# Kernel tuning notes

Hardware: AMD Instinct MI355X
Metric: run time of the kernel (lower is better)

## Reference

```python
import jax, jax.numpy as jnp
import numpy as np

K_NEIGH = 20
GROUPS = 4
KPTS = 9  # 3x3 deformable kernel
FH, FW = 240, 320


def _bn(x, p):
    # p: (4,C) rows = gamma, beta, running_mean, running_var ; x: (B,C,...)
    g, b, m, v = p[0], p[1], p[2], p[3]
    shp = (1, -1) + (1,) * (x.ndim - 2)
    return (x - m.reshape(shp)) * (g.reshape(shp) / jnp.sqrt(v.reshape(shp) + 1e-5)) + b.reshape(shp)


def _lrelu(x):
    return jnp.where(x >= 0, x, 0.2 * x)


def _c1x1(x, w):  # w: (Cout,Cin)
    return jnp.einsum('oc,bc...->bo...', w, x)


def _hswish(x):
    return x * jnp.clip(x + 3.0, 0.0, 6.0) / 6.0


def _coord_att(x, c1w, c1b, bnp, chw, chb, cww, cwb):
    B, C, H, W = x.shape
    ph = x.mean(axis=3, keepdims=True)                              # (B,C,H,1)
    pw = x.mean(axis=2, keepdims=True).transpose(0, 1, 3, 2)        # (B,C,W,1)
    y = jnp.concatenate([ph, pw], axis=2)                           # (B,C,H+W,1)
    y = _hswish(_bn(_c1x1(y, c1w) + c1b.reshape(1, -1, 1, 1), bnp))
    yh, yw = y[:, :, :H], y[:, :, H:]
    ah = jax.nn.sigmoid(_c1x1(yh, chw) + chb.reshape(1, -1, 1, 1))                         # (B,C,H,1)
    aw = jax.nn.sigmoid(_c1x1(yw.transpose(0, 1, 3, 2), cww) + cwb.reshape(1, -1, 1, 1))   # (B,C,1,W)
    return x * ah * aw


def _knn(x, k):
    xx = jnp.sum(x * x, axis=1)                     # (B,N)
    inner = jnp.einsum('bcn,bcm->bnm', x, x)
    pd = 2.0 * inner - xx[:, :, None] - xx[:, None, :]   # negative sq. distance
    return jax.lax.top_k(pd, k)[1]                  # (B,N,k)


def _graph_feature(x, k):
    B, C, N = x.shape
    idx = _knn(x, k)
    xt = x.transpose(0, 2, 1)                       # (B,N,C)
    nb = jax.vmap(lambda a, i: a[i])(xt, idx)       # (B,N,k,C)
    ctr = xt[:, :, None, :]
    f = jnp.concatenate([nb - ctr, jnp.broadcast_to(ctr, (B, N, k, C))], axis=3)
    return f.transpose(0, 3, 1, 2)                  # (B,2C,N,k)


def _dcnv4(x, off_w, off_b, val_w, val_b, out_w, out_b):
    B, C, H, W = x.shape
    Cg = C // GROUPS
    xh = x.transpose(0, 2, 3, 1)                    # (B,H,W,C)
    value = xh @ val_w + val_b
    om = (xh @ off_w + off_b).reshape(B, H, W, GROUPS, KPTS, 3)
    offs, mask = om[..., :2], om[..., 2]            # DCNv4: mask used un-normalized
    ky, kx = jnp.meshgrid(jnp.arange(-1, 2), jnp.arange(-1, 2), indexing='ij')
    kgrid = jnp.stack([kx.ravel(), ky.ravel()], -1).astype(x.dtype)      # (K,2) xy
    gy, gx = jnp.meshgrid(jnp.arange(H), jnp.arange(W), indexing='ij')
    base = jnp.stack([gx, gy], -1).astype(x.dtype)  # (H,W,2)
    loc = base[None, :, :, None, None, :] + kgrid + offs                 # (B,H,W,G,K,2)
    vflat = value.reshape(B, H * W, GROUPS, Cg)
    outs = []
    for g in range(GROUPS):
        lx = loc[:, :, :, g, :, 0]
        ly = loc[:, :, :, g, :, 1]                  # (B,H,W,K)
        x0 = jnp.floor(lx); y0 = jnp.floor(ly)
        wx = lx - x0; wy = ly - y0
        vg = vflat[:, :, g]                         # (B,HW,Cg)
        samp = jnp.zeros((B, H, W, KPTS, Cg), x.dtype)
        for yi, xi, w in ((y0, x0, (1 - wx) * (1 - wy)), (y0, x0 + 1, wx * (1 - wy)),
                          (y0 + 1, x0, (1 - wx) * wy), (y0 + 1, x0 + 1, wx * wy)):
            inb = (yi >= 0) & (yi < H) & (xi >= 0) & (xi < W)
            ii = (jnp.clip(yi, 0, H - 1) * W + jnp.clip(xi, 0, W - 1)).astype(jnp.int32)
            gathered = jax.vmap(lambda v, i: v[i])(vg, ii.reshape(B, -1)).reshape(B, H, W, KPTS, Cg)
            samp = samp + (w * inb)[..., None] * gathered
        outs.append(jnp.einsum('bhwk,bhwkc->bhwc', mask[:, :, :, g], samp))
    out = jnp.concatenate(outs, axis=-1) @ out_w + out_b
    return out.transpose(0, 3, 1, 2)


def setup_inputs() -> dict:
    key = jax.random.key(0)
    ks = jax.random.split(key, 24)
    B, N, IN_CH, FEAT_DIM = 2, 4096, 3, 128
    pc = jax.random.normal(ks[0], (B, 8, N), jnp.float32)
    v = jax.random.uniform(ks[1], (B, 1, N), jnp.float32, -240.0, 240.0)
    u = jax.random.uniform(ks[2], (B, 1, N), jnp.float32, -320.0, 320.0)
    pc = jnp.concatenate([v, u, pc[:, 2:]], axis=1)
    feat_s00 = jax.random.normal(ks[3], (B, IN_CH, 480, 640), jnp.float32)

    def w(k, shape, s=0.05):
        return jax.random.normal(k, shape, jnp.float32) * s

    def bn(c):
        return jnp.stack([jnp.ones(c), jnp.zeros(c), jnp.zeros(c), jnp.ones(c)]).astype(jnp.float32)

    OC = GROUPS * KPTS * 3
    return dict(
        pc_xyzrgb=pc, feat_s00=feat_s00,
        preconv_w=w(ks[4], (24, IN_CH, 3, 3)), preconv_b=jnp.zeros(24, jnp.float32),
        ca_c1_w=w(ks[5], (8, 24)), ca_c1_b=jnp.zeros(8, jnp.float32), ca_bn=bn(8),
        ca_ch_w=w(ks[6], (24, 8)), ca_ch_b=jnp.zeros(24, jnp.float32),
        ca_cw_w=w(ks[7], (24, 8)), ca_cw_b=jnp.zeros(24, jnp.float32),
        conv1_w=w(ks[8], (64, 64)), bn1=bn(64),
        conv2_w=w(ks[9], (64, 128)), bn2=bn(64),
        conv3_w=w(ks[10], (128, 128)), bn3=bn(128),
        lin4a_w=w(ks[11], (256, 256)), lin4b_w=w(ks[12], (256, 64)),
        dcn5_off_w=w(ks[13], (64, OC), 0.01), dcn5_off_b=jnp.zeros(OC, jnp.float32),
        dcn5_val_w=w(ks[14], (64, 64)), dcn5_val_b=jnp.zeros(64, jnp.float32),
        dcn5_out_w=w(ks[15], (64, 64)), dcn5_out_b=jnp.zeros(64, jnp.float32), bn5=bn(64),
        dcn6_off_w=w(ks[16], (64, OC), 0.01), dcn6_off_b=jnp.zeros(OC, jnp.float32),
        dcn6_val_w=w(ks[17], (64, 64)), dcn6_val_b=jnp.zeros(64, jnp.float32),
        dcn6_out_w=w(ks[18], (64, 64)), dcn6_out_b=jnp.zeros(64, jnp.float32), bn6=bn(64),
        conv7a_w=w(ks[19], (64, 64)), conv7b_w=w(ks[20], (FEAT_DIM, 64)),
    )


def reference(pc_xyzrgb, feat_s00, preconv_w, preconv_b, ca_c1_w, ca_c1_b, ca_bn, ca_ch_w, ca_ch_b,
              ca_cw_w, ca_cw_b, conv1_w, bn1, conv2_w, bn2, conv3_w, bn3, lin4a_w, lin4b_w,
              dcn5_off_w, dcn5_off_b, dcn5_val_w, dcn5_val_b, dcn5_out_w, dcn5_out_b, bn5,
              dcn6_off_w, dcn6_off_b, dcn6_val_w, dcn6_val_b, dcn6_out_w, dcn6_out_b, bn6,
              conv7a_w, conv7b_w):
    B, _, N = pc_xyzrgb.shape
    v = jnp.floor(pc_xyzrgb[:, 0] + 240.0).astype(jnp.int32).reshape(-1)
    u = jnp.floor(pc_xyzrgb[:, 1] + 320.0).astype(jnp.int32).reshape(-1)
    bi = jnp.repeat(jnp.arange(B, dtype=jnp.int32), N)
    # preConv: 3x3 conv + CoordAtt, then gather per-point 2D features
    fs1 = jax.lax.conv_general_dilated(feat_s00, preconv_w, (1, 1), 'SAME') + preconv_b.reshape(1, -1, 1, 1)
    fs1 = _coord_att(fs1, ca_c1_w, ca_c1_b, ca_bn, ca_ch_w, ca_ch_b, ca_cw_w, ca_cw_b)
    fs1 = fs1.transpose(0, 2, 3, 1)                                  # (B,480,640,24)
    feat_2d = fs1[bi, v, u].reshape(B, N, 24)
    feat_3d = jnp.concatenate([pc_xyzrgb.transpose(0, 2, 1), feat_2d], axis=2).transpose(0, 2, 1)  # (B,32,N)
    x = _lrelu(_bn(_c1x1(_graph_feature(feat_3d, K_NEIGH), conv1_w), bn1))
    x1 = x.max(axis=-1)                                              # (B,64,N)
    x = _lrelu(_bn(_c1x1(_graph_feature(x1, K_NEIGH), conv2_w), bn2))
    x2 = x.max(axis=-1)
    x = _lrelu(_bn(_c1x1(_graph_feature(x2, K_NEIGH), conv3_w), bn3))
    x3 = x.max(axis=-1)                                              # (B,128,N)
    x = jnp.concatenate([x1, x2, x3], axis=1).transpose(0, 2, 1)     # (B,N,256)
    x = (x @ lin4a_w) @ lin4b_w                                      # (B,N,64)
    fm = jnp.zeros((B, FH, FW, 64), x.dtype).at[bi, v // 2, u // 2].add(x.reshape(B * N, 64))
    fm = jax.nn.softmax(fm.transpose(0, 3, 1, 2), axis=1)            # (B,64,240,320)
    fm = _lrelu(_bn(_dcnv4(fm, dcn5_off_w, dcn5_off_b, dcn5_val_w, dcn5_val_b, dcn5_out_w, dcn5_out_b), bn5))
    fm = _lrelu(_bn(_dcnv4(fm, dcn6_off_w, dcn6_off_b, dcn6_val_w, dcn6_val_b, dcn6_out_w, dcn6_out_b), bn6))
    fm = _c1x1(_c1x1(fm, conv7a_w), conv7b_w)                        # (B,feat_dim,240,320)
    idx1 = jnp.stack([bi, v // 2, u // 2], axis=0)
    return fm, idx1
```

## Files before the change

kernel.cpp:

```cpp
#include <hip/hip_runtime.h>
#include <math.h>

#define B_    2
#define N_    4096
#define BN_   (B_*N_)
#define H0    480
#define W0    640
#define FH_   240
#define FW_   320
#define PIX_  (B_*FH_*FW_)
#define KNN_K 20

static const size_t OFF_RS   = 0;
static const size_t OFF_CS   = 2944;
static const size_t OFF_PH   = 6784;
static const size_t OFF_PW   = 29824;
static const size_t OFF_Y8   = 60544;
static const size_t OFF_AH   = 78464;
static const size_t OFF_AW   = 101504;
static const size_t OFF_VB   = 132224;
static const size_t OFF_UB   = 140416;
static const size_t OFF_F3D  = 148608;
static const size_t OFF_XX   = 410752;
static const size_t OFF_IDX  = 5661824;
static const size_t OFF_X1   = 5825664;
static const size_t OFF_X2   = 6349952;
static const size_t OFF_X3   = 6874240;
static const size_t OFF_T1   = 7922816;
static const size_t OFF_T2   = 7926912;
static const size_t OFF_T3   = 7935104;
static const size_t OFF_T7A  = 7951488;
static const size_t OFF_T7B  = 7955584;
static const size_t OFF_FMA  = 7963776;
static const size_t OFF_FMV  = 17794176;
static const size_t OFF_FMB  = 27624576;

__global__ void k_transpose(const float* __restrict__ w1, const float* __restrict__ w2,
                            const float* __restrict__ w3, const float* __restrict__ w7a,
                            const float* __restrict__ w7b,
                            float* __restrict__ t1, float* __restrict__ t2,
                            float* __restrict__ t3, float* __restrict__ t7a,
                            float* __restrict__ t7b) {
    int t = blockIdx.x * 256 + threadIdx.x;
    if (t < 4096) {
        int i = t >> 6, o = t & 63; t1[i*64+o] = w1[o*64+i];
    } else if (t < 12288) {
        int r = t - 4096; int i = r >> 6, o = r & 63; t2[i*64+o] = w2[o*128+i];
    } else if (t < 28672) {
        int r = t - 12288; int i = r >> 7, o = r & 127; t3[i*128+o] = w3[o*128+i];
    } else if (t < 32768) {
        int r = t - 28672; int c = r >> 6, o = r & 63; t7a[c*64+o] = w7a[o*64+c];
    } else if (t < 40960) {
        int r = t - 32768; int o = r >> 7, p = r & 127; t7b[o*128+p] = w7b[p*64+o];
    }
}

__global__ void k_sums(const float* __restrict__ img, float* __restrict__ cs,
                       float* __restrict__ rs) {
    int t = blockIdx.x * 256 + threadIdx.x;
    if (t < 6*W0) {
        int bc = t / W0, x = t % W0;
        const float* p = img + (size_t)bc * H0 * W0;
        float acc = 0.f;
        for (int h = 0; h < H0; ++h) acc += p[h * W0 + x];
        cs[bc * W0 + x] = acc;
    } else {
        int t2 = t - 6*W0;
        if (t2 < 6*H0) {
            int bc = t2 / H0, y = t2 % H0;
            const float* p = img + (size_t)bc * H0 * W0 + (size_t)y * W0;
            float acc = 0.f;
            for (int x = 0; x < W0; ++x) acc += p[x];
            rs[bc * H0 + y] = acc;
        }
    }
}

__global__ void k_phpw(const float* __restrict__ img, const float* __restrict__ rs,
                       const float* __restrict__ cs, const float* __restrict__ w,
                       const float* __restrict__ bias,
                       float* __restrict__ ph, float* __restrict__ pw) {
    int t = blockIdx.x * 256 + threadIdx.x;
    if (t < B_ * 24 * H0) {
        int h = t % H0; int bc = t / H0; int c = bc % 24; int b = bc / 24;
        float acc = 0.f;
        for (int ic = 0; ic < 3; ++ic)
            for (int dy = 0; dy < 3; ++dy) {
                int y = h + dy - 1;
                if ((unsigned)y >= (unsigned)H0) continue;
                float r = rs[(b*3+ic)*H0 + y];
                const float* row = img + (size_t)((b*3+ic)*H0 + y) * W0;
                float e0 = row[0], eL = row[W0-1];
                const float* wp = w + ((c*3+ic)*3+dy)*3;
                acc += wp[0]*(r - eL) + wp[1]*r + wp[2]*(r - e0);
            }
        ph[t] = bias[c] + acc / 640.0f;
    } else {
        int t2 = t - B_ * 24 * H0;
        if (t2 < B_ * 24 * W0) {
            int x = t2 % W0; int bc = t2 / W0; int c = bc % 24; int b = bc / 24;
            float acc = 0.f;
            for (int ic = 0; ic < 3; ++ic)
                for (int dx = 0; dx < 3; ++dx) {
                    int xx = x + dx - 1;
                    if ((unsigned)xx >= (unsigned)W0) continue;
                    float csv = cs[(b*3+ic)*W0 + xx];
                    const float* base = img + (size_t)(b*3+ic) * H0 * W0;
                    float top = base[xx];
                    float bot = base[(size_t)(H0-1)*W0 + xx];
                    const float* wp = w + ((c*3+ic)*3)*3 + dx;
                    acc += wp[0]*(csv - bot) + wp[3]*csv + wp[6]*(csv - top);
                }
            pw[t2] = bias[c] + acc / 480.0f;
        }
    }
}

__global__ void k_y8ahw(const float* __restrict__ ph, const float* __restrict__ pw,
                        const float* __restrict__ c1w, const float* __restrict__ c1b,
                        const float* __restrict__ bnp,
                        const float* __restrict__ chw, const float* __restrict__ chb,
                        const float* __restrict__ cww, const float* __restrict__ cwb,
                        float* __restrict__ ah, float* __restrict__ aw) {
    int t = blockIdx.x * 256 + threadIdx.x;
    if (t >= B_ * 1120) return;
    int pos = t % 1120; int b = t / 1120;
    float yv[24];
#pragma unroll
    for (int c = 0; c < 24; ++c)
        yv[c] = (pos < H0) ? ph[(b*24+c)*H0 + pos] : pw[(b*24+c)*W0 + (pos - H0)];
    float y8j[8];
#pragma unroll
    for (int j = 0; j < 8; ++j) {
        float s = c1b[j];
#pragma unroll
        for (int c = 0; c < 24; ++c) s = fmaf(c1w[j*24+c], yv[c], s);
        float g = bnp[j], be = bnp[8+j], m = bnp[16+j], va = bnp[24+j];
        float v = (s - m) * (g / sqrtf(va + 1e-5f)) + be;
        y8j[j] = v * fminf(fmaxf(v + 3.f, 0.f), 6.f) * (1.f/6.f);
    }
    if (pos < H0) {
#pragma unroll
        for (int c = 0; c < 24; ++c) {
            float s = chb[c];
#pragma unroll
            for (int j = 0; j < 8; ++j) s = fmaf(chw[c*8+j], y8j[j], s);
            ah[(b*24+c)*H0 + pos] = 1.f / (1.f + expf(-s));
        }
    } else {
#pragma unroll
        for (int c = 0; c < 24; ++c) {
            float s = cwb[c];
#pragma unroll
            for (int j = 0; j < 8; ++j) s = fmaf(cww[c*8+j], y8j[j], s);
            aw[(b*24+c)*W0 + (pos - H0)] = 1.f / (1.f + expf(-s));
        }
    }
}

__global__ void k_feat3d(const float* __restrict__ pc, const float* __restrict__ img,
                         const float* __restrict__ w, const float* __restrict__ bias,
                         const float* __restrict__ ah, const float* __restrict__ aw,
                         float* __restrict__ f3d, int* __restrict__ vbuf,
                         int* __restrict__ ubuf, float* __restrict__ idx_out) {
    int t = blockIdx.x * 256 + threadIdx.x;
    if (t >= BN_ * 32) return;
    int c = t & 31; int bn = t >> 5; int b = bn >> 12; int n = bn & (N_-1);
    float pv = pc[(b*8 + 0)*N_ + n];
    float pu = pc[(b*8 + 1)*N_ + n];
    int v = (int)floorf(pv + 240.f);
    int u = (int)floorf(pu + 320.f);
    float f;
    if (c < 8) {
        f = pc[(b*8 + c)*N_ + n];
    } else {
        int co = c - 8;
        float acc = bias[co];
        for (int ic = 0; ic < 3; ++ic)
            for (int dy = 0; dy < 3; ++dy) {
                int y = v + dy - 1;
                if ((unsigned)y >= (unsigned)H0) continue;
                for (int dx = 0; dx < 3; ++dx) {
                    int x = u + dx - 1;
                    if ((unsigned)x >= (unsigned)W0) continue;
                    acc = fmaf(w[((co*3+ic)*3+dy)*3+dx],
                               img[((size_t)(b*3+ic)*H0 + y)*W0 + x], acc);
                }
            }
        f = acc * ah[(b*24+co)*H0 + v] * aw[(b*24+co)*W0 + u];
    }
    f3d[(size_t)bn*32 + c] = f;
    if (c == 0) {
        vbuf[bn] = v; ubuf[bn] = u;
        idx_out[bn] = (float)b;
        idx_out[BN_ + bn] = (float)(v >> 1);
        idx_out[2*BN_ + bn] = (float)(u >> 1);
    }
}

template<int C>
__launch_bounds__(256, 2)
__global__ void k_dist(const float* __restrict__ X, float* __restrict__ pd, int b) {
    __shared__ float As[C*128];
    __shared__ float Bs[C*128];
    __shared__ float sXX[256];
    int tid = threadIdx.x;
    int t = blockIdx.x;
    int I = (int)((-1.0f + sqrtf(1.0f + 8.0f*(float)t)) * 0.5f);
    while ((I*(I+1))/2 > t) --I;
    while (((I+1)*(I+2))/2 <= t) ++I;
    int J = t - (I*(I+1))/2;
    {
        int r = tid >> 1, c0 = (tid & 1) * (C/2);
        const float* qa = X + ((size_t)(b*N_ + I*128 + r)) * C + c0;
        const float* ca = X + ((size_t)(b*N_ + J*128 + r)) * C + c0;
#pragma unroll
        for (int m = 0; m < C/8; ++m) {
            float4 va = *(const float4*)(qa + m*4);
            float4 vb = *(const float4*)(ca + m*4);
            int c = c0 + m*4;
            As[(c+0)*128+r]=va.x; As[(c+1)*128+r]=va.y; As[(c+2)*128+r]=va.z; As[(c+3)*128+r]=va.w;
            Bs[(c+0)*128+r]=vb.x; Bs[(c+1)*128+r]=vb.y; Bs[(c+2)*128+r]=vb.z; Bs[(c+3)*128+r]=vb.w;
        }
    }
    __syncthreads();
    int tx = tid & 15, ty = tid >> 4;
    float acc[8][8];
#pragma unroll
    for (int i=0;i<8;++i)
#pragma unroll
        for (int j=0;j<8;++j) acc[i][j]=0.f;
    for (int k = 0; k < C; ++k) {
        float4 a0 = *(const float4*)&As[k*128 + ty*8];
        float4 a1 = *(const float4*)&As[k*128 + ty*8 + 4];
        float4 b0 = *(const float4*)&Bs[k*128 + tx*8];
        float4 b1 = *(const float4*)&Bs[k*128 + tx*8 + 4];
        float av[8] = {a0.x,a0.y,a0.z,a0.w,a1.x,a1.y,a1.z,a1.w};
        float bv[8] = {b0.x,b0.y,b0.z,b0.w,b1.x,b1.y,b1.z,b1.w};
#pragma unroll
        for (int i = 0; i < 8; ++i)
#pragma unroll
            for (int j = 0; j < 8; ++j)
                acc[i][j] = fmaf(av[i], bv[j], acc[i][j]);
    }
    {
        float nacc = 0.f;
        if (tid < 128) {
            for (int c = 0; c < C; ++c) {
                float v = As[c*128 + tid];
                nacc = fmaf(v, v, nacc);
            }
        } else {
            int r = tid - 128;
            for (int c = 0; c < C; ++c) {
                float v = Bs[c*128 + r];
                nacc = fmaf(v, v, nacc);
            }
        }
        sXX[tid] = nacc;
    }
    __syncthreads();
    float xq[8], xc[8];
#pragma unroll
    for (int i = 0; i < 8; ++i) {
        xq[i] = sXX[ty*8 + i];
        xc[i] = sXX[128 + tx*8 + i];
    }
#pragma unroll
    for (int i = 0; i < 8; ++i) {
        int row = I*128 + ty*8 + i;
        float4 o0, o1;
        o0.x = 2.f*acc[i][0] - xq[i] - xc[0]; o0.y = 2.f*acc[i][1] - xq[i] - xc[1];
        o0.z = 2.f*acc[i][2] - xq[i] - xc[2]; o0.w = 2.f*acc[i][3] - xq[i] - xc[3];
        o1.x = 2.f*acc[i][4] - xq[i] - xc[4]; o1.y = 2.f*acc[i][5] - xq[i] - xc[5];
        o1.z = 2.f*acc[i][6] - xq[i] - xc[6]; o1.w = 2.f*acc[i][7] - xq[i] - xc[7];
        *(float4*)&pd[(size_t)row*N_ + J*128 + tx*8]     = o0;
        *(float4*)&pd[(size_t)row*N_ + J*128 + tx*8 + 4] = o1;
    }
    if (I != J) {
#pragma unroll
        for (int j = 0; j < 8; ++j) {
            int row = J*128 + tx*8 + j;
            float4 m0, m1;
            m0.x = 2.f*acc[0][j] - xc[j] - xq[0]; m0.y = 2.f*acc[1][j] - xc[j] - xq[1];
            m0.z = 2.f*acc[2][j] - xc[j] - xq[2]; m0.w = 2.f*acc[3][j] - xc[j] - xq[3];
            m1.x = 2.f*acc[4][j] - xc[j] - xq[4]; m1.y = 2.f*acc[5][j] - xc[j] - xq[5];
            m1.z = 2.f*acc[6][j] - xc[j] - xq[6]; m1.w = 2.f*acc[7][j] - xc[j] - xq[7];
            *(float4*)&pd[(size_t)row*N_ + I*128 + ty*8]     = m0;
            *(float4*)&pd[(size_t)row*N_ + I*128 + ty*8 + 4] = m1;
        }
    }
}

__launch_bounds__(256)
__global__ void k_select(const float* __restrict__ pd, int* __restrict__ idxb, int b) {
    int wv = threadIdx.x >> 6, lane = threadIdx.x & 63;
    int q = blockIdx.x * 4 + wv;
    const float* row = pd + (size_t)q * N_;
    float val[12]; int idx[12];
#pragma unroll
    for (int j = 0; j < 12; ++j) { val[j] = -INFINITY; idx[j] = 0x7fffffff; }
    for (int t = 0; t < N_ / 256; ++t) {
        float4 v4 = *(const float4*)(row + t * 256 + lane * 4);
        float vv[4] = {v4.x, v4.y, v4.z, v4.w};
#pragma unroll
        for (int j = 0; j < 4; ++j) {
            float v = vv[j];
            if (v > val[11]) {
                float cv = v; int cc = t * 256 + lane * 4 + j; bool ins = false;
#pragma unroll
                for (int s = 0; s < 12; ++s) {
                    bool sw = ins || (cv > val[s]);
                    if (sw) {
                        float tv = val[s]; val[s] = cv; cv = tv;
                        int ti = idx[s]; idx[s] = cc; cc = ti;
                        ins = true;
                    }
                }
            }
        }
    }
    int nb = 0;
    float hv = val[0]; int hi = idx[0];
#pragma unroll 1
    for (int slot = 0; slot < KNN_K; ++slot) {
        float wvv = hv; int wi = hi; int wl = lane;
#pragma unroll
        for (int off = 1; off < 64; off <<= 1) {
            float ov = __shfl_xor(wvv, off);
            int   oi = __shfl_xor(wi, off);
            int   ol = __shfl_xor(wl, off);
            bool take = (ov > wvv) || (ov == wvv && oi < wi);
            if (take) { wvv = ov; wi = oi; wl = ol; }
        }
        if (lane == slot) nb = wi;
        bool pop = (lane == wl);
#pragma unroll
        for (int s = 0; s < 11; ++s)
            if (pop) { val[s] = val[s+1]; idx[s] = idx[s+1]; }
        if (pop) { val[11] = -INFINITY; idx[11] = 0x7fffffff; }
        hv = val[0]; hi = idx[0];
    }
    if (lane < KNN_K) idxb[(size_t)(b * N_ + q) * KNN_K + lane] = nb;
}

template<int CIN, int COUT, int P>
__launch_bounds__(256, 2)
__global__ void edgeconv(const float* __restrict__ X, const int* __restrict__ idxb,
                         const float* __restrict__ wT, const float* __restrict__ bnp,
                         float* __restrict__ Y) {
    __shared__ float sctr[P][CIN];
    __shared__ float snb[P][KNN_K * CIN];
    int base = blockIdx.x * P;
    int tid = threadIdx.x;
    const int CIN4 = CIN / 4;
    if (tid < P * CIN4) {
        int p = tid / CIN4, i4 = tid % CIN4;
        ((float4*)sctr[p])[i4] = ((const float4*)&X[(size_t)(base + p) * CIN])[i4];
    }
    for (int j = tid; j < P * KNN_K * CIN4; j += 256) {
        int r = j / CIN4, i4 = j % CIN4;
        int p = r / KNN_K, k = r % KNN_K;
        int b = (base + p) / N_;
        int ni = idxb[(size_t)(base + p) * KNN_K + k];
        ((float4*)snb[p])[k * CIN4 + i4] =
            ((const float4*)&X[((size_t)b * N_ + ni) * CIN])[i4];
    }
    __syncthreads();
    int p = tid / COUT, o = tid % COUT;
    float wreg[CIN];
#pragma unroll
    for (int i = 0; i < CIN; ++i) wreg[i] = wT[i * COUT + o];
    float g = bnp[o], bb = bnp[COUT + o], m = bnp[2*COUT + o], va = bnp[3*COUT + o];
    float a = g / sqrtf(va + 1e-5f);
    float sh = bb - m * a;
    float accc = 0.f;
#pragma unroll
    for (int i = 0; i < CIN; ++i)
        accc = fmaf(wT[(CIN + i) * COUT + o] - wreg[i], sctr[p][i], accc);
    float mx = -INFINITY;
    for (int k = 0; k < KNN_K; ++k) {
        const float4* nb4 = (const float4*)&snb[p][k * CIN];
        float s = accc;
#pragma unroll
        for (int i4 = 0; i4 < CIN4; ++i4) {
            float4 v = nb4[i4];
            s = fmaf(wreg[4*i4+0], v.x, s);
            s = fmaf(wreg[4*i4+1], v.y, s);
            s = fmaf(wreg[4*i4+2], v.z, s);
            s = fmaf(wreg[4*i4+3], v.w, s);
        }
        float r = fmaf(s, a, sh);
        r = (r >= 0.f) ? r : 0.2f * r;
        mx = fmaxf(mx, r);
    }
    Y[(size_t)(base + p) * COUT + o] = mx;
}

__launch_bounds__(256)
__global__ void k_lin4(const float* __restrict__ x1, const float* __restrict__ x2,
                       const float* __restrict__ x3, const float* __restrict__ l4a,
                       const float* __restrict__ l4b, const int* __restrict__ vbuf,
                       const int* __restrict__ ubuf, float* __restrict__ fmA) {
    int p0 = blockIdx.x * 4; int tid = threadIdx.x;
    __shared__ float xc[4][256]; __shared__ float t1s[4][256];
    for (int j = tid; j < 1024; j += 256) {
        int p = j >> 8, i = j & 255;
        int bn = p0 + p;
        float v;
        if (i < 64)       v = x1[(size_t)bn*64 + i];
        else if (i < 128) v = x2[(size_t)bn*64 + i - 64];
        else              v = x3[(size_t)bn*128 + i - 128];
        xc[p][i] = v;
    }
    __syncthreads();
    float acc[4] = {0.f, 0.f, 0.f, 0.f};
#pragma unroll 8
    for (int i = 0; i < 256; ++i) {
        float wv = l4a[i*256 + tid];
#pragma unroll
        for (int p = 0; p < 4; ++p) acc[p] = fmaf(xc[p][i], wv, acc[p]);
    }
#pragma unroll
    for (int p = 0; p < 4; ++p) t1s[p][tid] = acc[p];
    __syncthreads();
    int o = tid & 63, pg = tid >> 6;
    float a2 = 0.f;
#pragma unroll 8
    for (int i = 0; i < 256; ++i) a2 = fmaf(t1s[pg][i], l4b[i*64 + o], a2);
    int bn = p0 + pg;
    int b = bn >> 12; int v = vbuf[bn] >> 1; int u = ubuf[bn] >> 1;
    atomicAdd(fmA + ((size_t)(b*FH_ + v)*FW_ + u)*64 + o, a2);
}

__launch_bounds__(256)
__global__ void k_dcnval(const float* __restrict__ in, const float* __restrict__ vw,
                         const float* __restrict__ vb, float* __restrict__ val,
                         float* __restrict__ smout, int do_sm) {
    __shared__ float sx[8][64];
    int tid = threadIdx.x;
    size_t base = (size_t)blockIdx.x * 512;
    if (tid < 128) ((float4*)sx)[tid] = *((const float4*)(in + base) + tid);
    __syncthreads();
    int o = tid & 63; int pg = tid >> 6;
    if (do_sm) {
        float x0 = sx[pg][o], x1 = sx[pg+4][o];
        float m0 = x0, m1 = x1;
        for (int off = 32; off > 0; off >>= 1) {
            m0 = fmaxf(m0, __shfl_xor(m0, off));
            m1 = fmaxf(m1, __shfl_xor(m1, off));
        }
        float e0 = expf(x0 - m0), e1 = expf(x1 - m1);
        float s0 = e0, s1 = e1;
        for (int off = 32; off > 0; off >>= 1) {
            s0 += __shfl_xor(s0, off);
            s1 += __shfl_xor(s1, off);
        }
        float r0 = e0 / s0, r1 = e1 / s1;
        smout[base + (size_t)pg*64 + o]     = r0;
        smout[base + (size_t)(pg+4)*64 + o] = r1;
        sx[pg][o] = r0; sx[pg+4][o] = r1;
        __syncthreads();
    }
    float bias = vb[o];
    float a0 = 0.f, a1 = 0.f;
#pragma unroll
    for (int i4 = 0; i4 < 16; ++i4) {
        float4 x0 = *(const float4*)&sx[pg][i4*4];
        float4 x1 = *(const float4*)&sx[pg+4][i4*4];
        float w0 = vw[(i4*4+0)*64 + o], w1 = vw[(i4*4+1)*64 + o];
        float w2 = vw[(i4*4+2)*64 + o], w3 = vw[(i4*4+3)*64 + o];
        a0 = fmaf(x0.x,w0,a0); a0 = fmaf(x0.y,w1,a0); a0 = fmaf(x0.z,w2,a0); a0 = fmaf(x0.w,w3,a0);
        a1 = fmaf(x1.x,w0,a1); a1 = fmaf(x1.y,w1,a1); a1 = fmaf(x1.z,w2,a1); a1 = fmaf(x1.w,w3,a1);
    }
    val[base + (size_t)pg*64 + o]     = a0 + bias;
    val[base + (size_t)(pg+4)*64 + o] = a1 + bias;
}

__launch_bounds__(256, 5)
__global__ void k_dcn64(const float* __restrict__ in, const float* __restrict__ val,
                        const float* __restrict__ ow, const float* __restrict__ ob,
                        const float* __restrict__ pwm, const float* __restrict__ pbm,
                        const float* __restrict__ bnp, float* __restrict__ out) {
    __shared__ float xT[64*36];
    __shared__ float somU[64*68];
    __shared__ float stapA[4][40][8];
    int tid = threadIdx.x;
    int blk = blockIdx.x;
    int b = blk / 2400;
    int hw0 = (blk % 2400) * 32;
    size_t pix0 = (size_t)b * (FH_*FW_) + hw0;

    {
        int px = tid >> 3, c0 = (tid & 7) * 8;
        const float* ip = in + (pix0 + px) * 64 + c0;
#pragma unroll
        for (int m = 0; m < 2; ++m) {
            float4 v = *(const float4*)(ip + m*4);
            int c = c0 + m*4;
            xT[(c+0)*36 + px] = v.x; xT[(c+1)*36 + px] = v.y;
            xT[(c+2)*36 + px] = v.z; xT[(c+3)*36 + px] = v.w;
        }
    }
    __builtin_amdgcn_wave_barrier();

    {
        int tx = tid & 15, ty = tid >> 4;
        int oadr[7];
#pragma unroll
        for (int j = 0; j < 7; ++j) {
            int o = tx + 16*j;
            oadr[j] = (o < 108) ? o : 107;
        }
        float acc[2][7];
#pragma unroll
        for (int i=0;i<2;++i)
#pragma unroll
            for (int j=0;j<7;++j) acc[i][j]=0.f;
        for (int c = 0; c < 64; ++c) {
            float2 a = *(const float2*)&xT[c*36 + ty*2];
            const float* owc = ow + c*108;
            float bv[7];
#pragma unroll
            for (int j = 0; j < 7; ++j) bv[j] = owc[oadr[j]];
#pragma unroll
            for (int j = 0; j < 7; ++j) {
                acc[0][j] = fmaf(a.x, bv[j], acc[0][j]);
                acc[1][j] = fmaf(a.y, bv[j], acc[1][j]);
            }
        }
#pragma unroll
        for (int j = 0; j < 7; ++j) {
            int o = tx + 16*j;
            if (o < 108) {
                float bias = ob[o];
                somU[(ty*2+0)*113 + o] = acc[0][j] + bias;
                somU[(ty*2+1)*113 + o] = acc[1][j] + bias;
            }
        }
    }
    __builtin_amdgcn_wave_barrier();

    int wv = tid >> 6, lane = tid & 63;
    const float* vb0 = val + (size_t)b * (FH_*FW_) * 64;
    int lane4 = lane << 2;
    for (int j = 0; j < 8; ++j) {
        int px = wv*8 + j;
        if (lane < 36) {
            int g = lane / 9, k = lane % 9;
            int hw = hw0 + px;
            int h = hw / FW_, w = hw % FW_;
            float lx = (float)(w + (k%3) - 1) + somU[px*113 + g*27 + k*3 + 0];
            float ly = (float)(h + (k/3) - 1) + somU[px*113 + g*27 + k*3 + 1];
            float msk = somU[px*113 + g*27 + k*3 + 2];
            float x0f = floorf(lx), y0f = floorf(ly);
            float wx = lx - x0f, wy = ly - y0f;
            int x0 = (int)x0f, y0 = (int)y0f;
            bool xi0 = (unsigned)x0 < (unsigned)FW_, xi1 = (unsigned)(x0+1) < (unsigned)FW_;
            bool yi0 = (unsigned)y0 < (unsigned)FH_, yi1 = (unsigned)(y0+1) < (unsigned)FH_;
            int x0c = min(max(x0, 0), FW_-1), x1c = min(max(x0+1, 0), FW_-1);
            int y0c = min(max(y0, 0), FH_-1), y1c = min(max(y0+1, 0), FH_-1);
            float4 fA, fW;
            fA.x = __int_as_float((y0c*FW_ + x0c) << 8);
            fA.y = __int_as_float((y0c*FW_ + x1c) << 8);
            fA.z = __int_as_float((y1c*FW_ + x0c) << 8);
            fA.w = __int_as_float((y1c*FW_ + x1c) << 8);
            fW.x = (xi0 && yi0) ? msk*(1.f-wx)*(1.f-wy) : 0.f;
            fW.y = (xi1 && yi0) ? msk*wx*(1.f-wy)       : 0.f;
            fW.z = (xi0 && yi1) ? msk*(1.f-wx)*wy       : 0.f;
            fW.w = (xi1 && yi1) ? msk*wx*wy             : 0.f;
            *(float4*)&stapA[wv][lane][0] = fA;
            *(float4*)&stapA[wv][lane][4] = fW;
        }
        __builtin_amdgcn_wave_barrier();
        {
            int g9 = (lane >> 4) * 9;
            float acc0 = 0.f, acc1 = 0.f;
#pragma unroll
            for (int k = 0; k < 9; ++k) {
                float4 A = *(const float4*)&stapA[wv][g9 + k][0];
                float4 W = *(const float4*)&stapA[wv][g9 + k][4];
                int a00 = __float_as_int(A.x) + lane4;
                int a01 = __float_as_int(A.y) + lane4;
                int a10 = __float_as_int(A.z) + lane4;
                int a11 = __float_as_int(A.w) + lane4;
                float v00 = *(const float*)((const char*)vb0 + (unsigned)a00);
                float v01 = *(const float*)((const char*)vb0 + (unsigned)a01);
                float v10 = *(const float*)((const char*)vb0 + (unsigned)a10);
                float v11 = *(const float*)((const char*)vb0 + (unsigned)a11);
                acc0 = fmaf(W.x, v00, acc0);
                acc1 = fmaf(W.y, v01, acc1);
                acc0 = fmaf(W.z, v10, acc0);
                acc1 = fmaf(W.w, v11, acc1);
            }
            xT[lane*36 + px] = acc0 + acc1;
        }
        __builtin_amdgcn_wave_barrier();
    }

    __syncthreads();
    for (int m = 0; m < 4; ++m) {
        int idx = tid + 256*m;
        int c = idx >> 4, o4 = (idx & 15) * 4;
        float4 v = *(const float4*)(pwm + c*64 + o4);
        *(float4*)&somU[c*68 + o4] = v;
    }
    __syncthreads();

    {
        int tx = tid & 15, ty = tid >> 4;
        float acc[2][4];
#pragma unroll
        for (int i=0;i<2;++i)
#pragma unroll
            for (int j=0;j<4;++j) acc[i][j]=0.f;
        for (int c = 0; c < 64; ++c) {
            float2 a = *(const float2*)&xT[c*36 + ty*2];
            float4 bb = *(const float4*)&somU[c*68 + tx*4];
            acc[0][0] = fmaf(a.x, bb.x, acc[0][0]);
            acc[0][1] = fmaf(a.x, bb.y, acc[0][1]);
            acc[0][2] = fmaf(a.x, bb.z, acc[0][2]);
            acc[0][3] = fmaf(a.x, bb.w, acc[0][3]);
            acc[1][0] = fmaf(a.y, bb.x, acc[1][0]);
            acc[1][1] = fmaf(a.y, bb.y, acc[1][1]);
            acc[1][2] = fmaf(a.y, bb.z, acc[1][2]);
            acc[1][3] = fmaf(a.y, bb.w, acc[1][3]);
        }
#pragma unroll
        for (int i = 0; i < 2; ++i) {
            int px = ty*2 + i;
            float vr[4];
#pragma unroll
            for (int jj = 0; jj < 4; ++jj) {
                int o = tx*4 + jj;
                float aa = acc[i][jj] + pbm[o];
                float g = bnp[o], be = bnp[64+o], m = bnp[128+o], va = bnp[192+o];
                float sc = g / sqrtf(va + 1e-5f);
                float r = (aa - m) * sc + be;
                vr[jj] = (r >= 0.f) ? r : 0.2f * r;
            }
            *(float4*)&out[(pix0 + px)*64 + tx*4] = make_float4(vr[0],vr[1],vr[2],vr[3]);
        }
    }
}

__launch_bounds__(256)
__global__ void k_conv7(const float* __restrict__ in, const float* __restrict__ w7aT,
                        const float* __restrict__ w7bT, float* __restrict__ out) {
    int blk = blockIdx.x;
    int b = blk / ((FH_*FW_)/16);
    int hw0 = (blk % ((FH_*FW_)/16)) * 16;
    int tid = threadIdx.x;
    __shared__ float sx[16][64];
    __shared__ float st[16][64];
    for (int j = tid; j < 1024; j += 256) {
        int p = j >> 6, c = j & 63;
        sx[p][c] = in[((size_t)(b*(FH_*FW_) + hw0 + p))*64 + c];
    }
    __syncthreads();
    {
        int o = tid & 63, p4 = tid >> 6;
        float acc[4] = {0.f, 0.f, 0.f, 0.f};
#pragma unroll 8
        for (int c = 0; c < 64; ++c) {
            float wv = w7aT[c*64 + o];
#pragma unroll
            for (int j = 0; j < 4; ++j) acc[j] = fmaf(sx[p4*4+j][c], wv, acc[j]);
        }
#pragma unroll
        for (int j = 0; j < 4; ++j) st[p4*4+j][o] = acc[j];
    }
    __syncthreads();
    {
        int po = tid >> 1, half = tid & 1;
        float acc[8] = {0.f};
#pragma unroll 8
        for (int c = 0; c < 64; ++c) {
            float wv = w7bT[c*128 + po];
#pragma unroll
            for (int j = 0; j < 8; ++j) acc[j] = fmaf(st[half*8+j][c], wv, acc[j]);
        }
        float* op = out + ((size_t)b*128 + po)*(FH_*FW_) + hw0 + half*8;
        *(float4*)op       = make_float4(acc[0], acc[1], acc[2], acc[3]);
        *(float4*)(op + 4) = make_float4(acc[4], acc[5], acc[6], acc[7]);
    }
}

extern "C" void kernel_launch(void* const* d_in, const int* in_sizes, int n_in,
                              void* d_out, int out_size, void* d_ws, size_t ws_size,
                              hipStream_t stream) {
    (void)in_sizes; (void)n_in; (void)out_size; (void)ws_size;
    const float* pc   = (const float*)d_in[0];
    const float* img  = (const float*)d_in[1];
    const float* pcw  = (const float*)d_in[2];
    const float* pcb  = (const float*)d_in[3];
    const float* c1w  = (const float*)d_in[4];
    const float* c1b  = (const float*)d_in[5];
    const float* cabn = (const float*)d_in[6];
    const float* chw  = (const float*)d_in[7];
    const float* chb  = (const float*)d_in[8];
    const float* cww  = (const float*)d_in[9];
    const float* cwb  = (const float*)d_in[10];
    const float* w1   = (const float*)d_in[11];
    const float* bn1  = (const float*)d_in[12];
    const float* w2   = (const float*)d_in[13];
    const float* bn2  = (const float*)d_in[14];
    const float* w3   = (const float*)d_in[15];
    const float* bn3  = (const float*)d_in[16];
    const float* l4a  = (const float*)d_in[17];
    const float* l4b  = (const float*)d_in[18];
    const float* d5ow = (const float*)d_in[19];
    const float* d5ob = (const float*)d_in[20];
    const float* d5vw = (const float*)d_in[21];
    const float* d5vb = (const float*)d_in[22];
    const float* d5pw = (const float*)d_in[23];
    const float* d5pb = (const float*)d_in[24];
    const float* bn5  = (const float*)d_in[25];
    const float* d6ow = (const float*)d_in[26];
    const float* d6ob = (const float*)d_in[27];
    const float* d6vw = (const float*)d_in[28];
    const float* d6vb = (const float*)d_in[29];
    const float* d6pw = (const float*)d_in[30];
    const float* d6pb = (const float*)d_in[31];
    const float* bn6  = (const float*)d_in[32];
    const float* w7a  = (const float*)d_in[33];
    const float* w7b  = (const float*)d_in[34];

    float* ws  = (float*)d_ws;
    float* out = (float*)d_out;

    float* rs  = ws + OFF_RS;   float* cs  = ws + OFF_CS;
    float* ph  = ws + OFF_PH;   float* pw  = ws + OFF_PW;
    float* ah  = ws + OFF_AH;   float* aw  = ws + OFF_AW;
    int*   vb  = (int*)(ws + OFF_VB);
    int*   ub  = (int*)(ws + OFF_UB);
    float* f3d = ws + OFF_F3D;
    int*   idxb = (int*)(ws + OFF_IDX);
    float* x1  = ws + OFF_X1;   float* x2  = ws + OFF_X2;  float* x3 = ws + OFF_X3;
    float* t1  = ws + OFF_T1;   float* t2  = ws + OFF_T2;  float* t3 = ws + OFF_T3;
    float* t7a = ws + OFF_T7A;  float* t7b = ws + OFF_T7B;
    float* fmA = ws + OFF_FMA;  float* fmV = ws + OFF_FMV; float* fmB = ws + OFF_FMB;
    float* pdb = ws + OFF_FMA;

    k_transpose<<<160, 256, 0, stream>>>(w1, w2, w3, w7a, w7b, t1, t2, t3, t7a, t7b);
    k_sums<<<27, 256, 0, stream>>>(img, cs, rs);
    k_phpw<<<210, 256, 0, stream>>>(img, rs, cs, pcw, pcb, ph, pw);
    k_y8ahw<<<9, 256, 0, stream>>>(ph, pw, c1w, c1b, cabn, chw, chb, cww, cwb, ah, aw);
    k_feat3d<<<(BN_*32)/256, 256, 0, stream>>>(pc, img, pcw, pcb, ah, aw, f3d, vb, ub,
                                               out + (size_t)B_*128*FH_*FW_);

    for (int b = 0; b < B_; ++b) {
        k_dist<32><<<528, 256, 0, stream>>>(f3d, pdb, b);
        k_select<<<N_/4, 256, 0, stream>>>(pdb, idxb, b);
    }
    edgeconv<32,64,4><<<BN_/4, 256, 0, stream>>>(f3d, idxb, t1, bn1, x1);
    for (int b = 0; b < B_; ++b) {
        k_dist<64><<<528, 256, 0, stream>>>(x1, pdb, b);
        k_select<<<N_/4, 256, 0, stream>>>(pdb, idxb, b);
    }
    edgeconv<64,64,4><<<BN_/4, 256, 0, stream>>>(x1, idxb, t2, bn2, x2);
    for (int b = 0; b < B_; ++b) {
        k_dist<64><<<528, 256, 0, stream>>>(x2, pdb, b);
        k_select<<<N_/4, 256, 0, stream>>>(pdb, idxb, b);
    }
    edgeconv<64,128,2><<<BN_/2, 256, 0, stream>>>(x2, idxb, t3, bn3, x3);

    hipMemsetAsync(fmA, 0, (size_t)PIX_ * 64 * sizeof(float), stream);
    k_lin4<<<BN_/4, 256, 0, stream>>>(x1, x2, x3, l4a, l4b, vb, ub, fmA);

    k_dcnval<<<PIX_/8, 256, 0, stream>>>(fmA, d5vw, d5vb, fmV, fmA, 1);
    k_dcn64<<<PIX_/32, 256, 0, stream>>>(fmA, fmV, d5ow, d5ob, d5pw, d5pb, bn5, fmB);
    k_dcnval<<<PIX_/8, 256, 0, stream>>>(fmB, d6vw, d6vb, fmV, fmB, 0);
    k_dcn64<<<PIX_/32, 256, 0, stream>>>(fmB, fmV, d6ow, d6ob, d6pw, d6pb, bn6, fmA);

    k_conv7<<<PIX_/16, 256, 0, stream>>>(fmA, t7a, t7b, out);
}
```

Before: 1.692 ms.

## Fuse kNN distance tiles with per-thread top-k and add a partial-list merge kernel

Replaces the full N×N distance-matrix write plus a separate row-wise top-k pass with a fused kernel. Each block computes 128-row distance tiles across a slice of columns, stages them in shared memory, and keeps a per-thread top-20 insertion list. A small merge kernel then combines the 8 partial lists per point. Both batches run in a single launch, which removes the large global pd traffic and the per-batch launches. In exchange it drops the symmetric-tile reuse, needs large shared memory at occupancy 1, and does redundant insertion-sort work in registers.

```diff
diff --git a/kernel.cpp b/kernel.cpp
--- a/kernel.cpp
+++ b/kernel.cpp
@@ -15,13 +15,11 @@
 static const size_t OFF_CS   = 2944;
 static const size_t OFF_PH   = 6784;
 static const size_t OFF_PW   = 29824;
-static const size_t OFF_Y8   = 60544;
 static const size_t OFF_AH   = 78464;
 static const size_t OFF_AW   = 101504;
 static const size_t OFF_VB   = 132224;
 static const size_t OFF_UB   = 140416;
 static const size_t OFF_F3D  = 148608;
-static const size_t OFF_XX   = 410752;
 static const size_t OFF_IDX  = 5661824;
 static const size_t OFF_X1   = 5825664;
 static const size_t OFF_X2   = 6349952;
@@ -34,6 +32,8 @@
 static const size_t OFF_FMA  = 7963776;
 static const size_t OFF_FMV  = 17794176;
 static const size_t OFF_FMB  = 27624576;
+static const size_t OFF_PVAL = OFF_FMA;
+static const size_t OFF_PIDX = OFF_FMA + 1310720;
 
 __global__ void k_transpose(const float* __restrict__ w1, const float* __restrict__ w2,
                             const float* __restrict__ w3, const float* __restrict__ w7a,
@@ -199,149 +199,164 @@
 }
 
 template<int C>
-__launch_bounds__(256, 2)
-__global__ void k_dist(const float* __restrict__ X, float* __restrict__ pd, int b) {
+__launch_bounds__(256, 1)
+__global__ void k_knn(const float* __restrict__ X, float* __restrict__ pval,
+                      int* __restrict__ pidx) {
     __shared__ float As[C*128];
     __shared__ float Bs[C*128];
-    __shared__ float sXX[256];
+    __shared__ float dt[128*132];
+    __shared__ float sxA[128];
+    __shared__ float sxB[128];
     int tid = threadIdx.x;
-    int t = blockIdx.x;
-    int I = (int)((-1.0f + sqrtf(1.0f + 8.0f*(float)t)) * 0.5f);
-    while ((I*(I+1))/2 > t) --I;
-    while (((I+1)*(I+2))/2 <= t) ++I;
-    int J = t - (I*(I+1))/2;
+    int blk = blockIdx.x;
+    int b  = blk >> 7;
+    int rem = blk & 127;
+    int I  = rem >> 2;
+    int js = rem & 3;
+
+    int sr = tid >> 1, sc0 = (tid & 1) * (C/2);
     {
-        int r = tid >> 1, c0 = (tid & 1) * (C/2);
-        const float* qa = X + ((size_t)(b*N_ + I*128 + r)) * C + c0;
-        const float* ca = X + ((size_t)(b*N_ + J*128 + r)) * C + c0;
+        const float* qa = X + ((size_t)(b*N_ + I*128 + sr)) * C + sc0;
 #pragma unroll
         for (int m = 0; m < C/8; ++m) {
             float4 va = *(const float4*)(qa + m*4);
-            float4 vb = *(const float4*)(ca + m*4);
-            int c = c0 + m*4;
-            As[(c+0)*128+r]=va.x; As[(c+1)*128+r]=va.y; As[(c+2)*128+r]=va.z; As[(c+3)*128+r]=va.w;
-            Bs[(c+0)*128+r]=vb.x; Bs[(c+1)*128+r]=vb.y; Bs[(c+2)*128+r]=vb.z; Bs[(c+3)*128+r]=vb.w;
-        }
-    }
-    __syncthreads();
+            int c = sc0 + m*4;
+            As[(c+0)*128+sr]=va.x; As[(c+1)*128+sr]=va.y;
+            As[(c+2)*128+sr]=va.z; As[(c+3)*128+sr]=va.w;
+        }
+    }
+
     int tx = tid & 15, ty = tid >> 4;
-    float acc[8][8];
-#pragma unroll
-    for (int i=0;i<8;++i)
-#pragma unroll
-        for (int j=0;j<8;++j) acc[i][j]=0.f;
-    for (int k = 0; k < C; ++k) {
-        float4 a0 = *(const float4*)&As[k*128 + ty*8];
-        float4 a1 = *(const float4*)&As[k*128 + ty*8 + 4];
-        float4 b0 = *(const float4*)&Bs[k*128 + tx*8];
-        float4 b1 = *(const float4*)&Bs[k*128 + tx*8 + 4];
-        float av[8] = {a0.x,a0.y,a0.z,a0.w,a1.x,a1.y,a1.z,a1.w};
-        float bv[8] = {b0.x,b0.y,b0.z,b0.w,b1.x,b1.y,b1.z,b1.w};
-#pragma unroll
-        for (int i = 0; i < 8; ++i)
-#pragma unroll
-            for (int j = 0; j < 8; ++j)
-                acc[i][j] = fmaf(av[i], bv[j], acc[i][j]);
-    }
-    {
-        float nacc = 0.f;
+    int row = tid >> 1, half = tid & 1;
+    float kv[KNN_K]; int ki[KNN_K];
+#pragma unroll
+    for (int s = 0; s < KNN_K; ++s) { kv[s] = -INFINITY; ki[s] = 0x7fffffff; }
+
+    for (int jt = 0; jt < 8; ++jt) {
+        int J = js*8 + jt;
+        {
+            const float* ca = X + ((size_t)(b*N_ + J*128 + sr)) * C + sc0;
+#pragma unroll
+            for (int m = 0; m < C/8; ++m) {
+                float4 vb = *(const float4*)(ca + m*4);
+                int c = sc0 + m*4;
+                Bs[(c+0)*128+sr]=vb.x; Bs[(c+1)*128+sr]=vb.y;
+                Bs[(c+2)*128+sr]=vb.z; Bs[(c+3)*128+sr]=vb.w;
+            }
+        }
+        __syncthreads();
         if (tid < 128) {
-            for (int c = 0; c < C; ++c) {
-                float v = As[c*128 + tid];
-                nacc = fmaf(v, v, nacc);
+            if (jt == 0) {
+                float nacc = 0.f;
+                for (int c = 0; c < C; ++c) {
+                    float v = As[c*128 + tid];
+                    nacc = fmaf(v, v, nacc);
+                }
+                sxA[tid] = nacc;
             }
         } else {
             int r = tid - 128;
+            float nacc = 0.f;
             for (int c = 0; c < C; ++c) {
                 float v = Bs[c*128 + r];
                 nacc = fmaf(v, v, nacc);
             }
-        }
-        sXX[tid] = nacc;
-    }
-    __syncthreads();
-    float xq[8], xc[8];
-#pragma unroll
-    for (int i = 0; i < 8; ++i) {
-        xq[i] = sXX[ty*8 + i];
-        xc[i] = sXX[128 + tx*8 + i];
-    }
-#pragma unroll
-    for (int i = 0; i < 8; ++i) {
-        int row = I*128 + ty*8 + i;
-        float4 o0, o1;
-        o0.x = 2.f*acc[i][0] - xq[i] - xc[0]; o0.y = 2.f*acc[i][1] - xq[i] - xc[1];
-        o0.z = 2.f*acc[i][2] - xq[i] - xc[2]; o0.w = 2.f*acc[i][3] - xq[i] - xc[3];
-        o1.x = 2.f*acc[i][4] - xq[i] - xc[4]; o1.y = 2.f*acc[i][5] - xq[i] - xc[5];
-        o1.z = 2.f*acc[i][6] - xq[i] - xc[6]; o1.w = 2.f*acc[i][7] - xq[i] - xc[7];
-        *(float4*)&pd[(size_t)row*N_ + J*128 + tx*8]     = o0;
-        *(float4*)&pd[(size_t)row*N_ + J*128 + tx*8 + 4] = o1;
-    }
-    if (I != J) {
-#pragma unroll
-        for (int j = 0; j < 8; ++j) {
-            int row = J*128 + tx*8 + j;
-            float4 m0, m1;
-            m0.x = 2.f*acc[0][j] - xc[j] - xq[0]; m0.y = 2.f*acc[1][j] - xc[j] - xq[1];
-            m0.z = 2.f*acc[2][j] - xc[j] - xq[2]; m0.w = 2.f*acc[3][j] - xc[j] - xq[3];
-            m1.x = 2.f*acc[4][j] - xc[j] - xq[4]; m1.y = 2.f*acc[5][j] - xc[j] - xq[5];
-            m1.z = 2.f*acc[6][j] - xc[j] - xq[6]; m1.w = 2.f*acc[7][j] - xc[j] - xq[7];
-            *(float4*)&pd[(size_t)row*N_ + I*128 + ty*8]     = m0;
-            *(float4*)&pd[(size_t)row*N_ + I*128 + ty*8 + 4] = m1;
-        }
-    }
-}
-
-__launch_bounds__(256)
-__global__ void k_select(const float* __restrict__ pd, int* __restrict__ idxb, int b) {
-    int wv = threadIdx.x >> 6, lane = threadIdx.x & 63;
-    int q = blockIdx.x * 4 + wv;
-    const float* row = pd + (size_t)q * N_;
-    float val[12]; int idx[12];
-#pragma unroll
-    for (int j = 0; j < 12; ++j) { val[j] = -INFINITY; idx[j] = 0x7fffffff; }
-    for (int t = 0; t < N_ / 256; ++t) {
-        float4 v4 = *(const float4*)(row + t * 256 + lane * 4);
-        float vv[4] = {v4.x, v4.y, v4.z, v4.w};
-#pragma unroll
-        for (int j = 0; j < 4; ++j) {
-            float v = vv[j];
-            if (v > val[11]) {
-                float cv = v; int cc = t * 256 + lane * 4 + j; bool ins = false;
-#pragma unroll
-                for (int s = 0; s < 12; ++s) {
-                    bool sw = ins || (cv > val[s]);
-                    if (sw) {
-                        float tv = val[s]; val[s] = cv; cv = tv;
-                        int ti = idx[s]; idx[s] = cc; cc = ti;
-                        ins = true;
+            sxB[r] = nacc;
+        }
+        __syncthreads();
+
+        float acc[8][8];
+#pragma unroll
+        for (int i=0;i<8;++i)
+#pragma unroll
+            for (int j=0;j<8;++j) acc[i][j]=0.f;
+        for (int k = 0; k < C; ++k) {
+            float4 a0 = *(const float4*)&As[k*128 + ty*8];
+            float4 a1 = *(const float4*)&As[k*128 + ty*8 + 4];
+            float4 b0 = *(const float4*)&Bs[k*128 + tx*8];
+            float4 b1 = *(const float4*)&Bs[k*128 + tx*8 + 4];
+            float av[8] = {a0.x,a0.y,a0.z,a0.w,a1.x,a1.y,a1.z,a1.w};
+            float bv[8] = {b0.x,b0.y,b0.z,b0.w,b1.x,b1.y,b1.z,b1.w};
+#pragma unroll
+            for (int i = 0; i < 8; ++i)
+#pragma unroll
+                for (int j = 0; j < 8; ++j)
+                    acc[i][j] = fmaf(av[i], bv[j], acc[i][j]);
+        }
+        float xq[8], xc[8];
+#pragma unroll
+        for (int i = 0; i < 8; ++i) {
+            xq[i] = sxA[ty*8 + i];
+            xc[i] = sxB[tx*8 + i];
+        }
+#pragma unroll
+        for (int i = 0; i < 8; ++i) {
+            float4 o0, o1;
+            o0.x = 2.f*acc[i][0] - xq[i] - xc[0]; o0.y = 2.f*acc[i][1] - xq[i] - xc[1];
+            o0.z = 2.f*acc[i][2] - xq[i] - xc[2]; o0.w = 2.f*acc[i][3] - xq[i] - xc[3];
+            o1.x = 2.f*acc[i][4] - xq[i] - xc[4]; o1.y = 2.f*acc[i][5] - xq[i] - xc[5];
+            o1.z = 2.f*acc[i][6] - xq[i] - xc[6]; o1.w = 2.f*acc[i][7] - xq[i] - xc[7];
+            *(float4*)&dt[(ty*8+i)*132 + tx*8]     = o0;
+            *(float4*)&dt[(ty*8+i)*132 + tx*8 + 4] = o1;
+        }
+        __syncthreads();
+        {
+            int gbase = J*128 + half*64;
+            const float* dr = &dt[row*132 + half*64];
+#pragma unroll
+            for (int i4 = 0; i4 < 16; ++i4) {
+                float4 v4 = *(const float4*)(dr + i4*4);
+                float vv[4] = {v4.x, v4.y, v4.z, v4.w};
+#pragma unroll
+                for (int e = 0; e < 4; ++e) {
+                    float v = vv[e];
+                    if (v > kv[KNN_K-1]) {
+                        float cv = v; int cc = gbase + i4*4 + e; bool ins = false;
+#pragma unroll
+                        for (int s = 0; s < KNN_K; ++s) {
+                            bool sw = ins || (cv > kv[s]);
+                            if (sw) {
+                                float tv = kv[s]; kv[s] = cv; cv = tv;
+                                int ti = ki[s]; ki[s] = cc; cc = ti;
+                                ins = true;
+                            }
+                        }
                     }
                 }
             }
         }
     }
-    int nb = 0;
-    float hv = val[0]; int hi = idx[0];
-#pragma unroll 1
-    for (int slot = 0; slot < KNN_K; ++slot) {
-        float wvv = hv; int wi = hi; int wl = lane;
-#pragma unroll
-        for (int off = 1; off < 64; off <<= 1) {
-            float ov = __shfl_xor(wvv, off);
-            int   oi = __shfl_xor(wi, off);
-            int   ol = __shfl_xor(wl, off);
-            bool take = (ov > wvv) || (ov == wvv && oi < wi);
-            if (take) { wvv = ov; wi = oi; wl = ol; }
-        }
-        if (lane == slot) nb = wi;
-        bool pop = (lane == wl);
-#pragma unroll
-        for (int s = 0; s < 11; ++s)
-            if (pop) { val[s] = val[s+1]; idx[s] = idx[s+1]; }
-        if (pop) { val[11] = -INFINITY; idx[11] = 0x7fffffff; }
-        hv = val[0]; hi = idx[0];
-    }
-    if (lane < KNN_K) idxb[(size_t)(b * N_ + q) * KNN_K + lane] = nb;
+    {
+        size_t o = (((size_t)(b*N_ + I*128 + row)) * 8 + (size_t)(js*2 + half)) * KNN_K;
+#pragma unroll
+        for (int s = 0; s < KNN_K; ++s) {
+            pval[o + s] = kv[s];
+            pidx[o + s] = ki[s];
+        }
+    }
+}
+
+__global__ void k_kmerge(const float* __restrict__ pval, const int* __restrict__ pidx,
+                         int* __restrict__ idxb) {
+    int t = blockIdx.x * 256 + threadIdx.x;
+    if (t >= BN_) return;
+    size_t base = (size_t)t * (8 * KNN_K);
+    int hp[8];
+#pragma unroll
+    for (int p = 0; p < 8; ++p) hp[p] = 0;
+    for (int s = 0; s < KNN_K; ++s) {
+        float bv = -INFINITY; int bi = 0x7fffffff; int bp = 0;
+#pragma unroll
+        for (int p = 0; p < 8; ++p) {
+            float v = pval[base + p*KNN_K + hp[p]];
+            int  ix = pidx[base + p*KNN_K + hp[p]];
+            bool take = (v > bv) || (v == bv && ix < bi);
+            if (take) { bv = v; bi = ix; bp = p; }
+        }
+        idxb[(size_t)t * KNN_K + s] = bi;
+#pragma unroll
+        for (int p = 0; p < 8; ++p) hp[p] += (bp == p) ? 1 : 0;
+    }
 }
 
 template<int CIN, int COUT, int P>
@@ -740,7 +755,8 @@
     float* t1  = ws + OFF_T1;   float* t2  = ws + OFF_T2;  float* t3 = ws + OFF_T3;
     float* t7a = ws + OFF_T7A;  float* t7b = ws + OFF_T7B;
     float* fmA = ws + OFF_FMA;  float* fmV = ws + OFF_FMV; float* fmB = ws + OFF_FMB;
-    float* pdb = ws + OFF_FMA;
+    float* pval = ws + OFF_PVAL;
+    int*   pidx = (int*)(ws + OFF_PIDX);
 
     k_transpose<<<160, 256, 0, stream>>>(w1, w2, w3, w7a, w7b, t1, t2, t3, t7a, t7b);
     k_sums<<<27, 256, 0, stream>>>(img, cs, rs);
@@ -749,20 +765,14 @@
     k_feat3d<<<(BN_*32)/256, 256, 0, stream>>>(pc, img, pcw, pcb, ah, aw, f3d, vb, ub,
                                                out + (size_t)B_*128*FH_*FW_);
 
-    for (int b = 0; b < B_; ++b) {
-        k_dist<32><<<528, 256, 0, stream>>>(f3d, pdb, b);
-        k_select<<<N_/4, 256, 0, stream>>>(pdb, idxb, b);
-    }
+    k_knn<32><<<256, 256, 0, stream>>>(f3d, pval, pidx);
+    k_kmerge<<<BN_/256, 256, 0, stream>>>(pval, pidx, idxb);
     edgeconv<32,64,4><<<BN_/4, 256, 0, stream>>>(f3d, idxb, t1, bn1, x1);
-    for (int b = 0; b < B_; ++b) {
-        k_dist<64><<<528, 256, 0, stream>>>(x1, pdb, b);
-        k_select<<<N_/4, 256, 0, stream>>>(pdb, idxb, b);
-    }
+    k_knn<64><<<256, 256, 0, stream>>>(x1, pval, pidx);
+    k_kmerge<<<BN_/256, 256, 0, stream>>>(pval, pidx, idxb);
     edgeconv<64,64,4><<<BN_/4, 256, 0, stream>>>(x1, idxb, t2, bn2, x2);
-    for (int b = 0; b < B_; ++b) {
-        k_dist<64><<<528, 256, 0, stream>>>(x2, pdb, b);
-        k_select<<<N_/4, 256, 0, stream>>>(pdb, idxb, b);
-    }
+    k_knn<64><<<256, 256, 0, stream>>>(x2, pval, pidx);
+    k_kmerge<<<BN_/256, 256, 0, stream>>>(pval, pidx, idxb);
     edgeconv<64,128,2><<<BN_/2, 256, 0, stream>>>(x2, idxb, t3, bn3, x3);
 
     hipMemsetAsync(fmA, 0, (size_t)PIX_ * 64 * sizeof(float), stream);
```

Result: slower. 4.665 ms (+175.7%).
